# Performance work log

Hardware: AMD Instinct MI355X
Metric: run time of the kernel (lower is better)

The kernel has to match this reference:

```python
import jax, jax.numpy as jnp
import numpy as np

DIM, H, D = 2048, 16, 128
D_C, D_CQ, D_ROPE = 512, 1536, 64
B, T = 2, 2048


def _rope(t, cos, sin):
    # t: [..., T, D_ROPE]; cos/sin: [T, D_ROPE//2] broadcast over leading dims
    h = D_ROPE // 2
    t1, t2 = t[..., :h], t[..., h:]
    return jnp.concatenate([t1 * cos - t2 * sin, t2 * cos + t1 * sin], axis=-1)


def setup_inputs() -> dict:
    key = jax.random.key(0)
    ks = jax.random.split(key, 10)
    init = lambda k, shp, fan: (jax.random.normal(k, shp, jnp.float32) / np.sqrt(fan).astype(np.float32))
    x = jax.random.normal(ks[0], (B, T, DIM), jnp.float32)
    # RoPE tables for d_rope//2 = 32 rotary channels
    inv_freq = 1.0 / (10000.0 ** (np.arange(0, D_ROPE // 2, dtype=np.float32) / (D_ROPE // 2)))
    ang = np.arange(T, dtype=np.float32)[:, None] * inv_freq[None, :]
    cos = jnp.asarray(np.cos(ang), jnp.float32)
    sin = jnp.asarray(np.sin(ang), jnp.float32)
    return {
        "x": x,
        "cos": cos,
        "sin": sin,
        "w_kv": init(ks[1], (DIM, D_C), DIM),          # kv_compress
        "w_kdec": init(ks[2], (D_C, H * D), D_C),       # k_decompress
        "w_vdec": init(ks[3], (D_C, H * D), D_C),       # v_decompress
        "w_qc": init(ks[4], (DIM, D_CQ), DIM),          # q_compress
        "w_qdec": init(ks[5], (D_CQ, H * D), D_CQ),     # q_decompress
        "w_krope": init(ks[6], (DIM, D_ROPE), DIM),     # k_rope_proj
        "w_qrope": init(ks[7], (DIM, D_ROPE), DIM),     # q_rope_proj
        "w_o": init(ks[8], (H * D, DIM), H * D),        # wo
    }


def reference(x, cos, sin, w_kv, w_kdec, w_vdec, w_qc, w_qdec, w_krope, w_qrope, w_o):
    Bx, Tx, _ = x.shape
    # latent compress -> decompress
    c_kv = x @ w_kv                                       # [B,T,d_c]
    k = (c_kv @ w_kdec).reshape(Bx, Tx, H, D).transpose(0, 2, 1, 3)  # [B,H,T,D]
    v = (c_kv @ w_vdec).reshape(Bx, Tx, H, D).transpose(0, 2, 1, 3)
    c_q = x @ w_qc
    q = (c_q @ w_qdec).reshape(Bx, Tx, H, D).transpose(0, 2, 1, 3)
    # RoPE branch: head-shared projections, rotated then broadcast across heads
    k_rope = _rope(x @ w_krope, cos, sin)                 # [B,T,d_rope]
    q_rope = _rope(x @ w_qrope, cos, sin)
    rope_dim = min(D_ROPE, D)
    qr = jnp.broadcast_to(q_rope[:, None, :, :rope_dim], (Bx, H, Tx, rope_dim))
    kr = jnp.broadcast_to(k_rope[:, None, :, :rope_dim], (Bx, H, Tx, rope_dim))
    q = jnp.concatenate([q[..., :-rope_dim], qr], axis=-1)
    k = jnp.concatenate([k[..., :-rope_dim], kr], axis=-1)
    # causal SDPA, scale = 1/sqrt(head_dim)
    scores = jnp.einsum("bhtd,bhsd->bhts", q, k) / np.float32(np.sqrt(D))
    causal = jnp.tril(jnp.ones((Tx, Tx), dtype=bool))
    scores = jnp.where(causal, scores, jnp.float32(-1e30))
    attn = jax.nn.softmax(scores, axis=-1)
    out = jnp.einsum("bhts,bhsd->bhtd", attn, v)
    out = out.transpose(0, 2, 1, 3).reshape(Bx, Tx, H * D)
    return out @ w_o
```

## Files before the change

### kernel.cpp

```cpp
#include <hip/hip_runtime.h>
#include <stdint.h>
#include <math.h>

#define B_    2
#define T_    2048
#define DIM_  2048
#define H_    16
#define DC_   512
#define DCQ_  1536
#define NROWS (B_*T_)

typedef unsigned short u16;
typedef __attribute__((ext_vector_type(8))) __bf16 bf16x8;
typedef __attribute__((ext_vector_type(4))) float  f32x4;
typedef __attribute__((ext_vector_type(8))) unsigned short u16x8;
typedef __attribute__((ext_vector_type(4))) float  f4v;

__device__ __forceinline__ u16 f2bf(float f){
  unsigned u = __float_as_uint(f);
  u += 0x7FFFu + ((u >> 16) & 1u);
  return (u16)(u >> 16);
}
__device__ __forceinline__ float bf2f(u16 h){ return __uint_as_float(((unsigned)h) << 16); }

__device__ __forceinline__ unsigned cvt_pk_bf16(float lo, float hi){
  unsigned r;
  asm("v_cvt_pk_bf16_f32 %0, %1, %2" : "=v"(r) : "v"(lo), "v"(hi));
  return r;
}

__device__ __forceinline__ void gld_lds16(const void* g, void* l){
  auto gp = reinterpret_cast<__attribute__((address_space(1))) unsigned int*>(
      reinterpret_cast<uintptr_t>(g));
  auto lp = reinterpret_cast<__attribute__((address_space(3))) unsigned int*>(
      reinterpret_cast<uintptr_t>(l));
  __builtin_amdgcn_global_load_lds(gp, lp, 16, 0, 0);
}

__device__ __forceinline__ f32x4 mfma16(bf16x8 a, bf16x8 b, f32x4 c){
  return __builtin_amdgcn_mfma_f32_16x16x32_bf16(a, b, c, 0, 0, 0);
}

__device__ __forceinline__ void vmwait0(){ asm volatile("s_waitcnt vmcnt(0)" ::: "memory"); }
__device__ __forceinline__ void vmwait8(){ asm volatile("s_waitcnt vmcnt(8)" ::: "memory"); }
__device__ __forceinline__ void barr(){ asm volatile("s_barrier" ::: "memory"); }

__global__ void k_detect(const u16* cosr, int* flag, int* ticket){
  if (threadIdx.x == 0) *flag = (cosr[0] == (u16)0x3F80u) ? 1 : 0;
  if (threadIdx.x < 128) ticket[threadIdx.x] = 0;
}

struct TDesc { const void* src; u16* dst; int srcStride, dstStride, cblk, nbx, blk0; };
struct TPack { TDesc d[8]; };
#define CONVBLK 8192

__global__ void k_prep(const void* __restrict__ xsrc, u16* __restrict__ x_bf,
                       TPack p, const int* flag){
  __shared__ u16 tile[64][72];
  const int bid = blockIdx.x;
  const int tid = threadIdx.x;
  const int f = *flag;
  if (bid < CONVBLK){
    int id = bid * 256 + tid;
    if (f){
      reinterpret_cast<uint2*>(x_bf)[id] = reinterpret_cast<const uint2*>(xsrc)[id];
    } else {
      f4v v = reinterpret_cast<const f4v*>(xsrc)[id];
      unsigned lo = (unsigned)f2bf(v.x) | ((unsigned)f2bf(v.y) << 16);
      unsigned hi = (unsigned)f2bf(v.z) | ((unsigned)f2bf(v.w) << 16);
      reinterpret_cast<uint2*>(x_bf)[id] = make_uint2(lo, hi);
    }
    return;
  }
  const int tb = bid - CONVBLK;
  int i = 0;
  #pragma unroll
  for (int k = 1; k < 8; ++k) if (tb >= p.d[k].blk0) i = k;
  const void* src = p.d[i].src;
  u16* dst = p.d[i].dst;
  const int srcStride = p.d[i].srcStride, dstStride = p.d[i].dstStride;
  const int rel = tb - p.d[i].blk0;
  const int bx = rel % p.d[i].nbx, by = rel / p.d[i].nbx;
  const int r0 = by << 6, c0 = bx * p.d[i].cblk;
  #pragma unroll
  for (int it = 0; it < 2; ++it){
    int task = (it << 8) + tid;
    int r = task >> 3, c8 = (task & 7) << 3;
    if (f){
      const u16* pp = (const u16*)src + (size_t)(r0 + r) * srcStride + c0 + c8;
      u16x8 v = *reinterpret_cast<const u16x8*>(pp);
      #pragma unroll
      for (int j = 0; j < 8; ++j) tile[r][c8 + j] = v[j];
    } else {
      const float* pp = (const float*)src + (size_t)(r0 + r) * srcStride + c0 + c8;
      f4v a = reinterpret_cast<const f4v*>(pp)[0];
      f4v b = reinterpret_cast<const f4v*>(pp)[1];
      tile[r][c8+0]=f2bf(a.x); tile[r][c8+1]=f2bf(a.y); tile[r][c8+2]=f2bf(a.z); tile[r][c8+3]=f2bf(a.w);
      tile[r][c8+4]=f2bf(b.x); tile[r][c8+5]=f2bf(b.y); tile[r][c8+6]=f2bf(b.z); tile[r][c8+7]=f2bf(b.w);
    }
  }
  __syncthreads();
  #pragma unroll
  for (int it = 0; it < 2; ++it){
    int task = (it << 8) + tid;
    int rr = task >> 3, cc8 = (task & 7) << 3;
    u16x8 v;
    #pragma unroll
    for (int j = 0; j < 8; ++j) v[j] = tile[cc8 + j][rr];
    *reinterpret_cast<u16x8*>(dst + (size_t)((bx << 6) + rr) * dstStride + r0 + cc8) = v;
  }
}

__global__ __launch_bounds__(256, 2) void k_gemm(
    const u16* __restrict__ A0, int lda0, const u16* __restrict__ Bt0, int K0,
    u16* __restrict__ C0, int ldc0, float os0,
    const u16* __restrict__ A1, int lda1, const u16* __restrict__ Bt1, int K1,
    u16* __restrict__ C1, int ldc1, float os1,
    int ysplit, int swz, void* outp, const int* flag){
  __shared__ alignas(16) u16 lds[32768];
  const int tid = threadIdx.x;
  const int wid = tid >> 6, lane = tid & 63;
  const int wr = wid >> 1, wc = wid & 1;
  const int l16 = lane & 15, g = lane >> 4;
  int lin = blockIdx.y * 32 + blockIdx.x;
  if (swz){
    const int q8 = (gridDim.x * gridDim.y) >> 3;
    lin = (lin & 7) * q8 + (lin >> 3);
  }
  const int m0 = (lin & 31) << 7;
  int nt = lin >> 5;
  const u16 *A, *Bt; u16* C; int lda, K, ldc; float oscale;
  if (nt < ysplit){ A = A0; lda = lda0; Bt = Bt0; K = K0; C = C0; ldc = ldc0; oscale = os0; }
  else { nt -= ysplit; A = A1; lda = lda1; Bt = Bt1; K = K1; C = C1; ldc = ldc1; oscale = os1; }
  const int n0 = nt << 7;
  const size_t Kz = (size_t)K;
  const int nkt = K >> 6;

  auto STAGE = [&](int kt, int bufn){
    const int kb = kt << 6;
    #pragma unroll
    for (int q = 0; q < 8; ++q){
      const int ht = q >> 2;
      const int cq = ((q & 3) << 8) + tid;
      const int Lb = cq << 4;
      const int row = Lb >> 7;
      const int colb = (Lb & 127) ^ ((row & 7) << 4);
      const u16* src = ht ? (Bt + (size_t)(n0 + row) * Kz + kb + (colb >> 1))
                          : (A  + (size_t)(m0 + row) * lda + kb + (colb >> 1));
      gld_lds16(src, &lds[bufn * 16384 + ht * 8192 + (cq << 3)]);
    }
  };

  f32x4 acc[4][4] = {};

  STAGE(0, 0);
  int buf = 0;

  for (int kt = 0; kt < nkt; ++kt){
    if (kt + 1 < nkt){ STAGE(kt + 1, buf ^ 1); vmwait8(); }
    else vmwait0();
    barr();
    bf16x8 af[2][4], bfr[2][4];
    #pragma unroll
    for (int ks = 0; ks < 2; ++ks){
      #pragma unroll
      for (int mi = 0; mi < 4; ++mi){
        int row = (wr << 6) + (mi << 4) + l16;
        int cb = ((ks << 6) + (g << 4)) ^ ((row & 7) << 4);
        af[ks][mi] = *reinterpret_cast<const bf16x8*>(&lds[buf * 16384 + (((row << 7) + cb) >> 1)]);
      }
      #pragma unroll
      for (int ni = 0; ni < 4; ++ni){
        int row = (wc << 6) + (ni << 4) + l16;
        int cb = ((ks << 6) + (g << 4)) ^ ((row & 7) << 4);
        bfr[ks][ni] = *reinterpret_cast<const bf16x8*>(&lds[buf * 16384 + 8192 + (((row << 7) + cb) >> 1)]);
      }
    }
    __builtin_amdgcn_s_setprio(1);
    #pragma unroll
    for (int ks = 0; ks < 2; ++ks)
      #pragma unroll
      for (int mi = 0; mi < 4; ++mi)
        #pragma unroll
        for (int ni = 0; ni < 4; ++ni)
          acc[mi][ni] = mfma16(af[ks][mi], bfr[ks][ni], acc[mi][ni]);
    __builtin_amdgcn_s_setprio(0);
    barr();
    buf ^= 1;
  }

  const int r4 = g << 2;
  const int f = flag ? *flag : 1;
  #pragma unroll
  for (int mi = 0; mi < 4; ++mi){
    int row = m0 + (wr << 6) + (mi << 4) + r4;
    #pragma unroll
    for (int ni = 0; ni < 4; ++ni){
      int col = n0 + (wc << 6) + (ni << 4) + l16;
      #pragma unroll
      for (int j = 0; j < 4; ++j){
        float v = acc[mi][ni][j] * oscale;
        if (outp){
          if (f) ((u16*)outp)[(size_t)(row + j) * ldc + col] = f2bf(v);
          else   ((float*)outp)[(size_t)(row + j) * ldc + col] = v;
        } else {
          C[(size_t)(row + j) * ldc + col] = f2bf(v);
        }
      }
    }
  }
}

__global__ void k_ropevt(const u16* __restrict__ xc, const void* __restrict__ cosp,
                         const void* __restrict__ sinp, const int* flag,
                         u16* __restrict__ krope, u16* __restrict__ qrope,
                         const u16* __restrict__ kvP, u16* __restrict__ vT){
  __shared__ u16 tile[64][72];
  if (blockIdx.x < 2048){
    int id = blockIdx.x * 256 + threadIdx.x;
    int row = id >> 7, c = id & 127;
    int t = row & (T_ - 1);
    int d = c & 63, i = d & 31;
    float cs, sn;
    if (*flag){ cs = bf2f(((const u16*)cosp)[t * 32 + i]); sn = bf2f(((const u16*)sinp)[t * 32 + i]); }
    else      { cs = ((const float*)cosp)[t * 32 + i];     sn = ((const float*)sinp)[t * 32 + i]; }
    int base = c & 64;
    float t1 = bf2f(xc[(size_t)row * 2304 + 2048 + base + i]);
    float t2 = bf2f(xc[(size_t)row * 2304 + 2048 + base + 32 + i]);
    float v = (d < 32) ? (t1 * cs - t2 * sn) : (t2 * cs + t1 * sn);
    if (c >= 64) v *= 0.12753139626374414f;
    ((c < 64) ? krope : qrope)[(size_t)row * 64 + d] = f2bf(v);
    return;
  }
  const int rel = blockIdx.x - 2048;
  const int t0 = (rel & 31) << 6, d0 = ((rel >> 5) & 1) << 6, bh = rel >> 6;
  const int b = bh >> 4, h = bh & 15;
  const int tid = threadIdx.x;
  #pragma unroll
  for (int i = 0; i < 2; ++i){
    int task = (i << 8) + tid;
    int r = task >> 3, c8 = (task & 7) << 3;
    const u16* p = kvP + (size_t)(b * T_ + t0 + r) * 3072 + 1024 + h * 128 + d0 + c8;
    u16x8 v = *reinterpret_cast<const u16x8*>(p);
    #pragma unroll
    for (int j = 0; j < 8; ++j) tile[r][c8 + j] = v[j];
  }
  __syncthreads();
  #pragma unroll
  for (int i = 0; i < 2; ++i){
    int task = (i << 8) + tid;
    int rr = task >> 3, cc8 = (task & 7) << 3;
    u16x8 v;
    #pragma unroll
    for (int j = 0; j < 8; ++j) v[j] = tile[cc8 + j][rr];
    *reinterpret_cast<u16x8*>(vT + ((size_t)bh * 128 + d0 + rr) * T_ + t0 + cc8) = v;
  }
}

__global__ __launch_bounds__(256, 2) void k_attn(const u16* __restrict__ qP,
                                                 const u16* __restrict__ kvP,
                                                 const u16* __restrict__ vT,
                                                 const u16* __restrict__ krope,
                                                 const u16* __restrict__ qrope,
                                                 u16* __restrict__ aout,
                                                 int* __restrict__ ticket){
  __shared__ alignas(16) u16 smem[32768];
  const int tid = threadIdx.x, wid = tid >> 6, lane = tid & 63;
  const int l16 = lane & 15, g = lane >> 4;
  const int lk = g << 3, r4 = g << 2;
  const int sw8 = (l16 & 7) << 3;
  const int xcd = blockIdx.x & 7;

  while (true){
    if (tid == 0) *(int*)&smem[0] = atomicAdd(&ticket[xcd << 4], 1);
    __syncthreads();
    const int it = *(const int*)&smem[0];
    __syncthreads();
    if (it >= 128) break;
    const int qt = 31 - (it >> 2);
    const int bh = (xcd << 2) + (it & 3), b = bh >> 4, h = bh & 15;
    const int q0 = qt << 6;
    const size_t bT = (size_t)b * T_;
    const u16* kvPb = kvP + bT * 3072 + (h << 6);
    const u16* krb  = krope + bT * 64;
    const u16* vTb  = vT + (size_t)bh * 128 * T_;
    const int qlo = q0 + (wid << 4);
    const int nkv = qt + 1;

    auto STAGE = [&](int buf, int k0){
      const int base = buf << 14;
      #pragma unroll
      for (int r = 0; r < 8; ++r){
        int c = (r << 8) + tid;
        const u16* src;
        if (r < 4){
          int row = c >> 4, cc = c & 15;
          int ccx = (cc & 8) | ((cc & 7) ^ (row & 7));
          int col0 = ccx << 3;
          src = (col0 < 64) ? (kvPb + (size_t)(k0 + row) * 3072 + col0)
                            : (krb  + (size_t)(k0 + row) * 64 + (col0 - 64));
        } else {
          int cv = c - 1024;
          int row = cv >> 3, cc = cv & 7;
          int ccx = cc ^ (row & 7);
          src = vTb + (size_t)row * T_ + k0 + (ccx << 3);
        }
        gld_lds16(src, &smem[base + (((r << 8) + (wid << 6)) << 3)]);
      }
    };

    bf16x8 qf[4];
    {
      size_t grow = bT + qlo + l16;
      #pragma unroll
      for (int ks = 0; ks < 4; ++ks){
        int d = (ks << 5) + lk;
        const u16* src = (ks < 2) ? (qP + grow * 1024 + (h << 6) + d)
                                  : (qrope + grow * 64 + (d - 64));
        qf[ks] = *reinterpret_cast<const bf16x8*>(src);
      }
    }
    f32x4 o[8] = {};
    float m = -3e38f, l = 0.f;

    STAGE(0, 0);
    __syncthreads();
    int cur = 0;

    for (int kv = 0; kv < nkv; ++kv){
      const int k0 = kv << 6;
      if (kv + 1 < nkv) STAGE(cur ^ 1, (kv + 1) << 6);
      const int kb = cur << 14;
      f32x4 s[4] = {};
      __builtin_amdgcn_s_setprio(1);
      #pragma unroll
      for (int ks = 0; ks < 4; ++ks){
        int colsw = ((ks << 5) + lk) ^ sw8;
        #pragma unroll
        for (int n = 0; n < 4; ++n){
          bf16x8 kf = *reinterpret_cast<const bf16x8*>(&smem[kb + ((n << 4) + l16) * 128 + colsw]);
          s[n] = mfma16(kf, qf[ks], s[n]);
        }
      }
      __builtin_amdgcn_s_setprio(0);
      if (k0 == q0){
        const int tq = qlo + l16;
        #pragma unroll
        for (int n = 0; n < 4; ++n)
          #pragma unroll
          for (int j = 0; j < 4; ++j)
            s[n][j] = (k0 + (n << 4) + r4 + j <= tq) ? s[n][j] : -3e38f;
      }
      float mx;
      {
        float a0 = fmaxf(fmaxf(s[0][0], s[0][1]), fmaxf(s[0][2], s[0][3]));
        float a1 = fmaxf(fmaxf(s[1][0], s[1][1]), fmaxf(s[1][2], s[1][3]));
        float a2 = fmaxf(fmaxf(s[2][0], s[2][1]), fmaxf(s[2][2], s[2][3]));
        float a3 = fmaxf(fmaxf(s[3][0], s[3][1]), fmaxf(s[3][2], s[3][3]));
        mx = fmaxf(fmaxf(a0, a1), fmaxf(a2, a3));
        mx = fmaxf(mx, __shfl_xor(mx, 16));
        mx = fmaxf(mx, __shfl_xor(mx, 32));
      }
      if (__ballot(mx > m + 8.f)){
        float mnew = fmaxf(m, mx);
        float alpha = exp2f(m - mnew);
        m = mnew; l *= alpha;
        #pragma unroll
        for (int j = 0; j < 4; ++j){
          float av = __shfl(alpha, r4 + j);
          #pragma unroll
          for (int db = 0; db < 8; ++db) o[db][j] *= av;
        }
      }
      unsigned w[4][2];
      float rs = 0.f;
      #pragma unroll
      for (int n = 0; n < 4; ++n)
        #pragma unroll
        for (int jh = 0; jh < 2; ++jh){
          float p0 = exp2f(s[n][2*jh]     - m);
          float p1 = exp2f(s[n][2*jh + 1] - m);
          rs += p0 + p1;
          w[n][jh] = cvt_pk_bf16(p0, p1);
        }
      rs += __shfl_xor(rs, 16);
      rs += __shfl_xor(rs, 32);
      l += rs;
      const int srcA = l16 + ((g & 1) << 5);
      const int srcB = srcA + 16;
      const bool hi = (g >= 2);
      bf16x8 pa[2];
      #pragma unroll
      for (int ks2 = 0; ks2 < 2; ++ks2){
        unsigned a0 = __shfl((int)w[2*ks2][0],     srcA);
        unsigned b0 = __shfl((int)w[2*ks2 + 1][0], srcA);
        unsigned a1 = __shfl((int)w[2*ks2][1],     srcA);
        unsigned b1 = __shfl((int)w[2*ks2 + 1][1], srcA);
        unsigned a2 = __shfl((int)w[2*ks2][0],     srcB);
        unsigned b2 = __shfl((int)w[2*ks2 + 1][0], srcB);
        unsigned a3 = __shfl((int)w[2*ks2][1],     srcB);
        unsigned b3 = __shfl((int)w[2*ks2 + 1][1], srcB);
        union { unsigned u[4]; bf16x8 v; } pk;
        pk.u[0] = hi ? b0 : a0;
        pk.u[1] = hi ? b1 : a1;
        pk.u[2] = hi ? b2 : a2;
        pk.u[3] = hi ? b3 : a3;
        pa[ks2] = pk.v;
      }
      __builtin_amdgcn_s_setprio(1);
      #pragma unroll
      for (int ks2 = 0; ks2 < 2; ++ks2){
        int colsw = ((ks2 << 5) + lk) ^ sw8;
        #pragma unroll
        for (int db = 0; db < 8; ++db){
          bf16x8 vb = *reinterpret_cast<const bf16x8*>(&smem[kb + 8192 + ((db << 4) + l16) * 64 + colsw]);
          o[db] = mfma16(pa[ks2], vb, o[db]);
        }
      }
      __builtin_amdgcn_s_setprio(0);
      __syncthreads();
      cur ^= 1;
    }
    #pragma unroll
    for (int j = 0; j < 4; ++j){
      float lv = __shfl(l, r4 + j);
      float rinv = 1.f / lv;
      const int tq = qlo + r4 + j;
      u16* dst = aout + (bT + tq) * 2048 + (h << 7) + l16;
      #pragma unroll
      for (int db = 0; db < 8; ++db)
        dst[db << 4] = f2bf(o[db][j] * rinv);
    }
  }
}

extern "C" void kernel_launch(void* const* d_in, const int* in_sizes, int n_in,
                              void* d_out, int out_size, void* d_ws, size_t ws_size,
                              hipStream_t stream){
  const void* x       = d_in[0];
  const void* cosp    = d_in[1];
  const void* sinp    = d_in[2];
  const void* w_kv    = d_in[3];
  const void* w_kdec  = d_in[4];
  const void* w_vdec  = d_in[5];
  const void* w_qc    = d_in[6];
  const void* w_qdec  = d_in[7];
  const void* w_krope = d_in[8];
  const void* w_qrope = d_in[9];
  const void* w_o     = d_in[10];

  char* ws = (char*)d_ws;
  size_t off = 0;
  auto alloc = [&](size_t bytes){ void* p = ws + off; off += (bytes + 255) & ~(size_t)255; return p; };
  int* flag     = (int*)alloc(256);
  int* ticket   = (int*)alloc(1024);
  u16* x_bf     = (u16*)alloc((size_t)NROWS * DIM_ * 2);
  u16* w_c1T    = (u16*)alloc((size_t)2304 * DIM_ * 2);
  u16* w_kvdT   = (u16*)alloc((size_t)3072 * DC_ * 2);
  u16* w_qdPT   = (u16*)alloc((size_t)1024 * DCQ_ * 2);
  u16* w_oT     = (u16*)alloc((size_t)DIM_ * DIM_ * 2);
  u16* xc       = (u16*)alloc((size_t)NROWS * 2304 * 2);
  u16* qP       = (u16*)alloc((size_t)NROWS * 1024 * 2);
  u16* kvP      = (u16*)alloc((size_t)NROWS * 3072 * 2);
  u16* krope    = (u16*)alloc((size_t)NROWS * 64 * 2);
  u16* qrope    = (u16*)alloc((size_t)NROWS * 64 * 2);
  u16* vT       = (u16*)alloc((size_t)32 * 128 * T_ * 2);
  u16* aout     = (u16*)alloc((size_t)NROWS * DIM_ * 2);
  (void)in_sizes; (void)n_in; (void)out_size; (void)ws_size;

  const float SC2 = 0.12753139626374414f;

  hipLaunchKernelGGL(k_detect, dim3(1), dim3(128), 0, stream, (const u16*)cosp, flag, ticket);

  TPack tp;
  tp.d[0] = { w_kv,    w_c1T,                        512,  2048, 64,  8,  0    };
  tp.d[1] = { w_qc,    w_c1T + (size_t)512 * 2048,   1536, 2048, 64,  24, 256  };
  tp.d[2] = { w_krope, w_c1T + (size_t)2048 * 2048,  64,   2048, 64,  1,  1024 };
  tp.d[3] = { w_qrope, w_c1T + (size_t)2112 * 2048,  64,   2048, 64,  1,  1056 };
  tp.d[4] = { w_kdec,  w_kvdT,                       2048, 512,  128, 16, 1088 };
  tp.d[5] = { w_vdec,  w_kvdT + (size_t)1024 * 512,  2048, 512,  64,  32, 1216 };
  tp.d[6] = { w_qdec,  w_qdPT,                       2048, 1536, 128, 16, 1472 };
  tp.d[7] = { w_o,     w_oT,                         2048, 2048, 64,  32, 1856 };
  hipLaunchKernelGGL(k_prep, dim3(CONVBLK + 2880), dim3(256), 0, stream, x, x_bf, tp, flag);

  hipLaunchKernelGGL(k_gemm, dim3(32, 18), dim3(256), 0, stream,
                     x_bf, DIM_, w_c1T, DIM_, xc, 2304, 1.0f,
                     x_bf, DIM_, w_c1T, DIM_, xc, 2304, 1.0f,
                     18, 1, (void*)nullptr, (const int*)nullptr);
  hipLaunchKernelGGL(k_gemm, dim3(32, 32), dim3(256), 0, stream,
                     xc + 512, 2304, w_qdPT, DCQ_, qP, 1024, SC2,
                     xc, 2304, w_kvdT, DC_, kvP, 3072, 1.0f,
                     8, 0, (void*)nullptr, (const int*)nullptr);
  hipLaunchKernelGGL(k_ropevt, dim3(4096), dim3(256), 0, stream,
                     xc, cosp, sinp, flag, krope, qrope, kvP, vT);
  hipLaunchKernelGGL(k_attn, dim3(512), dim3(256), 0, stream,
                     qP, kvP, vT, krope, qrope, aout, ticket);
  hipLaunchKernelGGL(k_gemm, dim3(32, 16), dim3(256), 0, stream,
                     aout, DIM_, w_oT, DIM_, (u16*)nullptr, DIM_, 1.0f,
                     aout, DIM_, w_oT, DIM_, (u16*)nullptr, DIM_, 1.0f,
                     16, 1, d_out, (const int*)flag);
}
```

Measured before the change: 253.7 us.

## Use 128-row query tiles with 512-thread attention blocks; skip bf16 x copy

The attention kernel moves to 512-thread blocks, each covering a 128-query tile with 8 waves that share every staged K/V tile. This halves the number of work items, and the staging loop now uses four rounds over 512 threads. Waves whose queries lie entirely before a KV tile skip its compute but still join the barrier. Separately, when the input is already bf16, the first GEMM reads x directly instead of a copy made by the prep kernel, removing that pass; in the fp32 case the conversion still runs. Larger blocks may reduce occupancy and add load imbalance on the diagonal tiles.

```diff
diff --git a/kernel.cpp b/kernel.cpp
--- a/kernel.cpp
+++ b/kernel.cpp
@@ -61,15 +61,12 @@
   const int tid = threadIdx.x;
   const int f = *flag;
   if (bid < CONVBLK){
+    if (f) return;
     int id = bid * 256 + tid;
-    if (f){
-      reinterpret_cast<uint2*>(x_bf)[id] = reinterpret_cast<const uint2*>(xsrc)[id];
-    } else {
-      f4v v = reinterpret_cast<const f4v*>(xsrc)[id];
-      unsigned lo = (unsigned)f2bf(v.x) | ((unsigned)f2bf(v.y) << 16);
-      unsigned hi = (unsigned)f2bf(v.z) | ((unsigned)f2bf(v.w) << 16);
-      reinterpret_cast<uint2*>(x_bf)[id] = make_uint2(lo, hi);
-    }
+    f4v v = reinterpret_cast<const f4v*>(xsrc)[id];
+    unsigned lo = (unsigned)f2bf(v.x) | ((unsigned)f2bf(v.y) << 16);
+    unsigned hi = (unsigned)f2bf(v.z) | ((unsigned)f2bf(v.w) << 16);
+    reinterpret_cast<uint2*>(x_bf)[id] = make_uint2(lo, hi);
     return;
   }
   const int tb = bid - CONVBLK;
@@ -116,7 +113,8 @@
     u16* __restrict__ C0, int ldc0, float os0,
     const u16* __restrict__ A1, int lda1, const u16* __restrict__ Bt1, int K1,
     u16* __restrict__ C1, int ldc1, float os1,
-    int ysplit, int swz, void* outp, const int* flag){
+    int ysplit, int swz, void* outp, const int* flag,
+    const u16* __restrict__ alt0, const u16* __restrict__ alt1){
   __shared__ alignas(16) u16 lds[32768];
   const int tid = threadIdx.x;
   const int wid = tid >> 6, lane = tid & 63;
@@ -129,9 +127,11 @@
   }
   const int m0 = (lin & 31) << 7;
   int nt = lin >> 5;
-  const u16 *A, *Bt; u16* C; int lda, K, ldc; float oscale;
-  if (nt < ysplit){ A = A0; lda = lda0; Bt = Bt0; K = K0; C = C0; ldc = ldc0; oscale = os0; }
-  else { nt -= ysplit; A = A1; lda = lda1; Bt = Bt1; K = K1; C = C1; ldc = ldc1; oscale = os1; }
+  const u16 *A, *Bt, *alt; u16* C; int lda, K, ldc; float oscale;
+  if (nt < ysplit){ A = A0; lda = lda0; Bt = Bt0; K = K0; C = C0; ldc = ldc0; oscale = os0; alt = alt0; }
+  else { nt -= ysplit; A = A1; lda = lda1; Bt = Bt1; K = K1; C = C1; ldc = ldc1; oscale = os1; alt = alt1; }
+  const int f = flag ? *flag : 1;
+  if (alt && f) A = alt;
   const int n0 = nt << 7;
   const size_t Kz = (size_t)K;
   const int nkt = K >> 6;
@@ -190,7 +190,6 @@
   }
 
   const int r4 = g << 2;
-  const int f = flag ? *flag : 1;
   #pragma unroll
   for (int mi = 0; mi < 4; ++mi){
     int row = m0 + (wr << 6) + (mi << 4) + r4;
@@ -257,7 +256,7 @@
   }
 }
 
-__global__ __launch_bounds__(256, 2) void k_attn(const u16* __restrict__ qP,
+__global__ __launch_bounds__(512, 2) void k_attn(const u16* __restrict__ qP,
                                                  const u16* __restrict__ kvP,
                                                  const u16* __restrict__ vT,
                                                  const u16* __restrict__ krope,
@@ -276,24 +275,25 @@
     __syncthreads();
     const int it = *(const int*)&smem[0];
     __syncthreads();
-    if (it >= 128) break;
-    const int qt = 31 - (it >> 2);
+    if (it >= 64) break;
+    const int qt = 15 - (it >> 2);
     const int bh = (xcd << 2) + (it & 3), b = bh >> 4, h = bh & 15;
-    const int q0 = qt << 6;
+    const int q0 = qt << 7;
     const size_t bT = (size_t)b * T_;
     const u16* kvPb = kvP + bT * 3072 + (h << 6);
     const u16* krb  = krope + bT * 64;
     const u16* vTb  = vT + (size_t)bh * 128 * T_;
     const int qlo = q0 + (wid << 4);
-    const int nkv = qt + 1;
+    const int qhi = qlo + 15;
+    const int nkv = (qt << 1) + 2;
 
     auto STAGE = [&](int buf, int k0){
       const int base = buf << 14;
       #pragma unroll
-      for (int r = 0; r < 8; ++r){
-        int c = (r << 8) + tid;
+      for (int r = 0; r < 4; ++r){
+        int c = (r << 9) + tid;
         const u16* src;
-        if (r < 4){
+        if (r < 2){
           int row = c >> 4, cc = c & 15;
           int ccx = (cc & 8) | ((cc & 7) ^ (row & 7));
           int col0 = ccx << 3;
@@ -305,7 +305,7 @@
           int ccx = cc ^ (row & 7);
           src = vTb + (size_t)row * T_ + k0 + (ccx << 3);
         }
-        gld_lds16(src, &smem[base + (((r << 8) + (wid << 6)) << 3)]);
+        gld_lds16(src, &smem[base + (c << 3)]);
       }
     };
 
@@ -330,94 +330,96 @@
     for (int kv = 0; kv < nkv; ++kv){
       const int k0 = kv << 6;
       if (kv + 1 < nkv) STAGE(cur ^ 1, (kv + 1) << 6);
-      const int kb = cur << 14;
-      f32x4 s[4] = {};
-      __builtin_amdgcn_s_setprio(1);
-      #pragma unroll
-      for (int ks = 0; ks < 4; ++ks){
-        int colsw = ((ks << 5) + lk) ^ sw8;
+      if (k0 <= qhi){
+        const int kb = cur << 14;
+        f32x4 s[4] = {};
+        __builtin_amdgcn_s_setprio(1);
         #pragma unroll
-        for (int n = 0; n < 4; ++n){
-          bf16x8 kf = *reinterpret_cast<const bf16x8*>(&smem[kb + ((n << 4) + l16) * 128 + colsw]);
-          s[n] = mfma16(kf, qf[ks], s[n]);
-        }
-      }
-      __builtin_amdgcn_s_setprio(0);
-      if (k0 == q0){
-        const int tq = qlo + l16;
+        for (int ks = 0; ks < 4; ++ks){
+          int colsw = ((ks << 5) + lk) ^ sw8;
+          #pragma unroll
+          for (int n = 0; n < 4; ++n){
+            bf16x8 kf = *reinterpret_cast<const bf16x8*>(&smem[kb + ((n << 4) + l16) * 128 + colsw]);
+            s[n] = mfma16(kf, qf[ks], s[n]);
+          }
+        }
+        __builtin_amdgcn_s_setprio(0);
+        if (k0 + 63 > qlo){
+          const int tq = qlo + l16;
+          #pragma unroll
+          for (int n = 0; n < 4; ++n)
+            #pragma unroll
+            for (int j = 0; j < 4; ++j)
+              s[n][j] = (k0 + (n << 4) + r4 + j <= tq) ? s[n][j] : -3e38f;
+        }
+        float mx;
+        {
+          float a0 = fmaxf(fmaxf(s[0][0], s[0][1]), fmaxf(s[0][2], s[0][3]));
+          float a1 = fmaxf(fmaxf(s[1][0], s[1][1]), fmaxf(s[1][2], s[1][3]));
+          float a2 = fmaxf(fmaxf(s[2][0], s[2][1]), fmaxf(s[2][2], s[2][3]));
+          float a3 = fmaxf(fmaxf(s[3][0], s[3][1]), fmaxf(s[3][2], s[3][3]));
+          mx = fmaxf(fmaxf(a0, a1), fmaxf(a2, a3));
+          mx = fmaxf(mx, __shfl_xor(mx, 16));
+          mx = fmaxf(mx, __shfl_xor(mx, 32));
+        }
+        if (__ballot(mx > m + 8.f)){
+          float mnew = fmaxf(m, mx);
+          float alpha = exp2f(m - mnew);
+          m = mnew; l *= alpha;
+          #pragma unroll
+          for (int j = 0; j < 4; ++j){
+            float av = __shfl(alpha, r4 + j);
+            #pragma unroll
+            for (int db = 0; db < 8; ++db) o[db][j] *= av;
+          }
+        }
+        unsigned w[4][2];
+        float rs = 0.f;
         #pragma unroll
         for (int n = 0; n < 4; ++n)
           #pragma unroll
-          for (int j = 0; j < 4; ++j)
-            s[n][j] = (k0 + (n << 4) + r4 + j <= tq) ? s[n][j] : -3e38f;
+          for (int jh = 0; jh < 2; ++jh){
+            float p0 = exp2f(s[n][2*jh]     - m);
+            float p1 = exp2f(s[n][2*jh + 1] - m);
+            rs += p0 + p1;
+            w[n][jh] = cvt_pk_bf16(p0, p1);
+          }
+        rs += __shfl_xor(rs, 16);
+        rs += __shfl_xor(rs, 32);
+        l += rs;
+        const int srcA = l16 + ((g & 1) << 5);
+        const int srcB = srcA + 16;
+        const bool hi = (g >= 2);
+        bf16x8 pa[2];
+        #pragma unroll
+        for (int ks2 = 0; ks2 < 2; ++ks2){
+          unsigned a0 = __shfl((int)w[2*ks2][0],     srcA);
+          unsigned b0 = __shfl((int)w[2*ks2 + 1][0], srcA);
+          unsigned a1 = __shfl((int)w[2*ks2][1],     srcA);
+          unsigned b1 = __shfl((int)w[2*ks2 + 1][1], srcA);
+          unsigned a2 = __shfl((int)w[2*ks2][0],     srcB);
+          unsigned b2 = __shfl((int)w[2*ks2 + 1][0], srcB);
+          unsigned a3 = __shfl((int)w[2*ks2][1],     srcB);
+          unsigned b3 = __shfl((int)w[2*ks2 + 1][1], srcB);
+          union { unsigned u[4]; bf16x8 v; } pk;
+          pk.u[0] = hi ? b0 : a0;
+          pk.u[1] = hi ? b1 : a1;
+          pk.u[2] = hi ? b2 : a2;
+          pk.u[3] = hi ? b3 : a3;
+          pa[ks2] = pk.v;
+        }
+        __builtin_amdgcn_s_setprio(1);
+        #pragma unroll
+        for (int ks2 = 0; ks2 < 2; ++ks2){
+          int colsw = ((ks2 << 5) + lk) ^ sw8;
+          #pragma unroll
+          for (int db = 0; db < 8; ++db){
+            bf16x8 vb = *reinterpret_cast<const bf16x8*>(&smem[(cur << 14) + 8192 + ((db << 4) + l16) * 64 + colsw]);
+            o[db] = mfma16(pa[ks2], vb, o[db]);
+          }
+        }
+        __builtin_amdgcn_s_setprio(0);
       }
-      float mx;
-      {
-        float a0 = fmaxf(fmaxf(s[0][0], s[0][1]), fmaxf(s[0][2], s[0][3]));
-        float a1 = fmaxf(fmaxf(s[1][0], s[1][1]), fmaxf(s[1][2], s[1][3]));
-        float a2 = fmaxf(fmaxf(s[2][0], s[2][1]), fmaxf(s[2][2], s[2][3]));
-        float a3 = fmaxf(fmaxf(s[3][0], s[3][1]), fmaxf(s[3][2], s[3][3]));
-        mx = fmaxf(fmaxf(a0, a1), fmaxf(a2, a3));
-        mx = fmaxf(mx, __shfl_xor(mx, 16));
-        mx = fmaxf(mx, __shfl_xor(mx, 32));
-      }
-      if (__ballot(mx > m + 8.f)){
-        float mnew = fmaxf(m, mx);
-        float alpha = exp2f(m - mnew);
-        m = mnew; l *= alpha;
-        #pragma unroll
-        for (int j = 0; j < 4; ++j){
-          float av = __shfl(alpha, r4 + j);
-          #pragma unroll
-          for (int db = 0; db < 8; ++db) o[db][j] *= av;
-        }
-      }
-      unsigned w[4][2];
-      float rs = 0.f;
-      #pragma unroll
-      for (int n = 0; n < 4; ++n)
-        #pragma unroll
-        for (int jh = 0; jh < 2; ++jh){
-          float p0 = exp2f(s[n][2*jh]     - m);
-          float p1 = exp2f(s[n][2*jh + 1] - m);
-          rs += p0 + p1;
-          w[n][jh] = cvt_pk_bf16(p0, p1);
-        }
-      rs += __shfl_xor(rs, 16);
-      rs += __shfl_xor(rs, 32);
-      l += rs;
-      const int srcA = l16 + ((g & 1) << 5);
-      const int srcB = srcA + 16;
-      const bool hi = (g >= 2);
-      bf16x8 pa[2];
-      #pragma unroll
-      for (int ks2 = 0; ks2 < 2; ++ks2){
-        unsigned a0 = __shfl((int)w[2*ks2][0],     srcA);
-        unsigned b0 = __shfl((int)w[2*ks2 + 1][0], srcA);
-        unsigned a1 = __shfl((int)w[2*ks2][1],     srcA);
-        unsigned b1 = __shfl((int)w[2*ks2 + 1][1], srcA);
-        unsigned a2 = __shfl((int)w[2*ks2][0],     srcB);
-        unsigned b2 = __shfl((int)w[2*ks2 + 1][0], srcB);
-        unsigned a3 = __shfl((int)w[2*ks2][1],     srcB);
-        unsigned b3 = __shfl((int)w[2*ks2 + 1][1], srcB);
-        union { unsigned u[4]; bf16x8 v; } pk;
-        pk.u[0] = hi ? b0 : a0;
-        pk.u[1] = hi ? b1 : a1;
-        pk.u[2] = hi ? b2 : a2;
-        pk.u[3] = hi ? b3 : a3;
-        pa[ks2] = pk.v;
-      }
-      __builtin_amdgcn_s_setprio(1);
-      #pragma unroll
-      for (int ks2 = 0; ks2 < 2; ++ks2){
-        int colsw = ((ks2 << 5) + lk) ^ sw8;
-        #pragma unroll
-        for (int db = 0; db < 8; ++db){
-          bf16x8 vb = *reinterpret_cast<const bf16x8*>(&smem[kb + 8192 + ((db << 4) + l16) * 64 + colsw]);
-          o[db] = mfma16(pa[ks2], vb, o[db]);
-        }
-      }
-      __builtin_amdgcn_s_setprio(0);
       __syncthreads();
       cur ^= 1;
     }
@@ -486,17 +488,20 @@
   hipLaunchKernelGGL(k_gemm, dim3(32, 18), dim3(256), 0, stream,
                      x_bf, DIM_, w_c1T, DIM_, xc, 2304, 1.0f,
                      x_bf, DIM_, w_c1T, DIM_, xc, 2304, 1.0f,
-                     18, 1, (void*)nullptr, (const int*)nullptr);
+                     18, 1, (void*)nullptr, (const int*)flag,
+                     (const u16*)x, (const u16*)x);
   hipLaunchKernelGGL(k_gemm, dim3(32, 32), dim3(256), 0, stream,
                      xc + 512, 2304, w_qdPT, DCQ_, qP, 1024, SC2,
                      xc, 2304, w_kvdT, DC_, kvP, 3072, 1.0f,
-                     8, 0, (void*)nullptr, (const int*)nullptr);
+                     8, 0, (void*)nullptr, (const int*)nullptr,
+                     (const u16*)nullptr, (const u16*)nullptr);
   hipLaunchKernelGGL(k_ropevt, dim3(4096), dim3(256), 0, stream,
                      xc, cosp, sinp, flag, krope, qrope, kvP, vT);
-  hipLaunchKernelGGL(k_attn, dim3(512), dim3(256), 0, stream,
+  hipLaunchKernelGGL(k_attn, dim3(256), dim3(512), 0, stream,
                      qP, kvP, vT, krope, qrope, aout, ticket);
   hipLaunchKernelGGL(k_gemm, dim3(32, 16), dim3(256), 0, stream,
                      aout, DIM_, w_oT, DIM_, (u16*)nullptr, DIM_, 1.0f,
                      aout, DIM_, w_oT, DIM_, (u16*)nullptr, DIM_, 1.0f,
-                     16, 1, d_out, (const int*)flag);
-}
+                     16, 1, d_out, (const int*)flag,
+                     (const u16*)nullptr, (const u16*)nullptr);
+}
```

New measurement: 249.8 us. About the same (-1.5%).
